# Kernel optimization log

Hardware: AMD Instinct MI355X
Metric: run time of the kernel (lower is better)

Reference implementation:

```python
import jax, jax.numpy as jnp
import numpy as np

B, E, Hh, Ww = 32, 256, 64, 64
HID = 256

def setup_inputs() -> dict:
    key = jax.random.key(0)
    k1, k2, k3 = jax.random.split(key, 3)
    x = jax.random.normal(k1, (B, E, Hh, Ww), dtype=jnp.float32)
    # 1x1 conv weights flattened to [out_ch, in_ch]
    Wqkv = jax.random.normal(k2, (1 + 2 * HID, E), dtype=jnp.float32) * (1.0 / np.sqrt(E))
    bqkv = jnp.zeros((1 + 2 * HID,), dtype=jnp.float32)
    Wout = jax.random.normal(k3, (E, HID), dtype=jnp.float32) * (1.0 / np.sqrt(HID))
    bout = jnp.zeros((E,), dtype=jnp.float32)
    return {"x": x, "Wqkv": Wqkv, "bqkv": bqkv, "Wout": Wout, "bout": bout}

def reference(x, Wqkv, bqkv, Wout, bout):
    hid = HID
    # 1x1 conv == channel-wise matmul: [B,C,H,W] x [O,C] -> [B,O,H,W]
    qkv = jnp.einsum('bchw,oc->bohw', x, Wqkv) + bqkv[None, :, None, None]
    query = qkv[:, :1]               # [B,1,H,W]
    key_t = qkv[:, 1:1 + hid]        # [B,hid,H,W]
    value = qkv[:, 1 + hid:]         # [B,hid,H,W]
    # softmax over the last (width) axis; dropout is identity at eval
    context_scores = jax.nn.softmax(query, axis=-1)
    # softmax-weighted sum over width -> [B,hid,H,1]
    context_vector = jnp.sum(key_t * context_scores, axis=-1, keepdims=True)
    # relu gate on value, broadcast context over width
    gated = jax.nn.relu(value) * context_vector  # [B,hid,H,W]
    out = jnp.einsum('bchw,oc->bohw', gated, Wout) + bout[None, :, None, None]
    return out
```

## Files before the change

kernel.cpp:

```cpp
#include <hip/hip_runtime.h>

#define BB   32
#define EE   256
#define HH   64
#define WW   64
#define HIDN 256

typedef short bf16x8 __attribute__((ext_vector_type(8)));
typedef float f32x4  __attribute__((ext_vector_type(4)));

__device__ __forceinline__ float ubf(unsigned short u) {
  return __uint_as_float(((unsigned)u) << 16);
}
__device__ __forceinline__ unsigned f2bf(float f) {
  unsigned u = __float_as_uint(f);
  u += 0x7fffu + ((u >> 16) & 1u);
  return u >> 16;
}

__device__ __forceinline__ int xt_idx(int w, int c) {
  return (w << 8) + ((((c >> 3) ^ (w & 7)) << 3) | (c & 7));
}

__global__ __launch_bounds__(256) void prep_weights(
    const float* __restrict__ Wqkv, const float* __restrict__ Wout,
    unsigned short* __restrict__ ws)
{
  const int t = blockIdx.x * 256 + threadIdx.x;
  const int which = t >> 13;
  const int r = t & 8191;
  const int m = r >> 5, k8 = r & 31, k0 = k8 * 8;
  const float* src = which ? (Wout + m * HIDN + k0)
                           : (Wqkv + (1 + HIDN + m) * EE + k0);
  unsigned short* dst = ws + which * 131072;
  float4 a = *(const float4*)src;
  float4 bq = *(const float4*)(src + 4);
  float v[8] = {a.x, a.y, a.z, a.w, bq.x, bq.y, bq.z, bq.w};
  const int mt = m >> 4, ks = k8 >> 2, lane = (m & 15) + ((k8 & 3) << 4);
  const int base = ((mt * 8 + ks) * 2) * 64 * 8 + lane * 8;
  __align__(16) unsigned short hs[8], ls[8];
  #pragma unroll
  for (int i = 0; i < 8; ++i) {
    unsigned h = f2bf(v[i]);
    hs[i] = (unsigned short)h;
    ls[i] = (unsigned short)f2bf(v[i] - ubf((unsigned short)h));
  }
  *(uint4*)&dst[base]       = *(const uint4*)hs;
  *(uint4*)&dst[base + 512] = *(const uint4*)ls;
}

__device__ __forceinline__ void mfma_gemm(
    const bf16x8* __restrict__ Wp,
    const unsigned short* __restrict__ Xhp,
    const unsigned short* __restrict__ Xlp,
    const int wid, const int lane, f32x4 acc[4][4])
{
  const int l15 = lane & 15;
  const int kb  = (lane >> 4) * 8;
  #pragma unroll
  for (int ks = 0; ks < 8; ++ks) {
    bf16x8 bhf[4], blf[4];
    #pragma unroll
    for (int ni = 0; ni < 4; ++ni) {
      const int w  = ni * 16 + l15;
      const int c0 = ks * 32 + kb;
      bhf[ni] = *(const bf16x8*)&Xhp[xt_idx(w, c0)];
      blf[ni] = *(const bf16x8*)&Xlp[xt_idx(w, c0)];
    }
    bf16x8 ahf[4], alf[4];
    #pragma unroll
    for (int mi = 0; mi < 4; ++mi) {
      const int fb = ((wid * 4 + mi) * 8 + ks) * 2;
      ahf[mi] = Wp[fb * 64 + lane];
      alf[mi] = Wp[(fb + 1) * 64 + lane];
    }
    #pragma unroll
    for (int mi = 0; mi < 4; ++mi) {
      #pragma unroll
      for (int ni = 0; ni < 4; ++ni) {
        acc[mi][ni] = __builtin_amdgcn_mfma_f32_16x16x32_bf16(ahf[mi], bhf[ni], acc[mi][ni], 0, 0, 0);
        acc[mi][ni] = __builtin_amdgcn_mfma_f32_16x16x32_bf16(ahf[mi], blf[ni], acc[mi][ni], 0, 0, 0);
        acc[mi][ni] = __builtin_amdgcn_mfma_f32_16x16x32_bf16(alf[mi], bhf[ni], acc[mi][ni], 0, 0, 0);
      }
    }
  }
}

__global__ __launch_bounds__(256, 2) void sep_attn_mfma(
    const float* __restrict__ x, const float* __restrict__ Wqkv,
    const float* __restrict__ bqkv, const float* __restrict__ bout,
    float* __restrict__ out, const unsigned short* __restrict__ wsp)
{
  __shared__ __align__(16) unsigned short Xh[64 * 256];
  __shared__ __align__(16) unsigned short Xl[64 * 256];
  __shared__ __align__(16) float qpart[256];
  __shared__ __align__(16) float ss[64];
  __shared__ __align__(16) float xbar_s[EE];
  __shared__ __align__(16) float cvs[EE];
  __shared__ __align__(16) float sbv[EE];
  __shared__ __align__(16) float sbout[EE];

  const int tid  = threadIdx.x;
  const int lane = tid & 63;
  const int wid  = tid >> 6;
  const int bh = blockIdx.x;
  const int b  = bh >> 6;
  const int h  = bh & 63;
  const int gbase = (b * EE) * 4096 + h * 64;

  {
    const int c = tid;
    const float* xp = x + gbase + c * 4096;
    sbv[tid]   = bqkv[1 + HIDN + tid];
    sbout[tid] = bout[tid];
    #pragma unroll
    for (int f = 0; f < 16; ++f) {
      float4 xv = *(const float4*)&xp[f * 4];
      float vv[4] = {xv.x, xv.y, xv.z, xv.w};
      #pragma unroll
      for (int j = 0; j < 4; ++j) {
        const int w = f * 4 + j;
        unsigned hu = f2bf(vv[j]);
        Xh[xt_idx(w, c)] = (unsigned short)hu;
        Xl[xt_idx(w, c)] = (unsigned short)f2bf(vv[j] - ubf((unsigned short)hu));
      }
    }
  }
  __syncthreads();

  {
    const int w = tid & 63, cg = tid >> 6;
    const float* wq = Wqkv + cg * 64;
    float q = 0.f;
    #pragma unroll
    for (int f = 0; f < 8; ++f) {
      const int c0 = cg * 64 + f * 8;
      bf16x8 hv = *(const bf16x8*)&Xh[xt_idx(w, c0)];
      bf16x8 lv = *(const bf16x8*)&Xl[xt_idx(w, c0)];
      float4 wa = *(const float4*)&wq[f * 8];
      float4 wb = *(const float4*)&wq[f * 8 + 4];
      float wf[8] = {wa.x, wa.y, wa.z, wa.w, wb.x, wb.y, wb.z, wb.w};
      #pragma unroll
      for (int e = 0; e < 8; ++e)
        q = fmaf(wf[e], ubf((unsigned short)hv[e]) + ubf((unsigned short)lv[e]), q);
    }
    qpart[tid] = q;
  }
  __syncthreads();

  if (tid < 64) {
    float q = qpart[tid] + qpart[64 + tid] + qpart[128 + tid] + qpart[192 + tid] + bqkv[0];
    float m = q;
    #pragma unroll
    for (int off = 32; off; off >>= 1) m = fmaxf(m, __shfl_xor(m, off));
    float e = expf(q - m);
    float s = e;
    #pragma unroll
    for (int off = 32; off; off >>= 1) s += __shfl_xor(s, off);
    ss[tid] = e / s;
  }
  __syncthreads();

  {
    const int c = tid;
    float a = 0.f;
    #pragma unroll
    for (int f = 0; f < 16; ++f) {
      float4 sv = *(const float4*)&ss[f * 4];
      float4 xv = *(const float4*)&x[gbase + c * 4096 + f * 4];
      a += sv.x * xv.x + sv.y * xv.y + sv.z * xv.z + sv.w * xv.w;
    }
    xbar_s[c] = a;
  }
  __syncthreads();

  {
    const int c = tid;
    const float* wk = Wqkv + (1 + c) * EE;
    float a = 0.f;
    #pragma unroll 8
    for (int f = 0; f < 64; ++f) {
      float4 wv = *(const float4*)&wk[f * 4];
      float4 xb = *(const float4*)&xbar_s[f * 4];
      a += wv.x * xb.x + wv.y * xb.y + wv.z * xb.z + wv.w * xb.w;
    }
    cvs[c] = a + bqkv[1 + c];
  }

  f32x4 acc[4][4];
  #pragma unroll
  for (int mi = 0; mi < 4; ++mi)
    #pragma unroll
    for (int ni = 0; ni < 4; ++ni) {
      acc[mi][ni][0] = 0.f; acc[mi][ni][1] = 0.f;
      acc[mi][ni][2] = 0.f; acc[mi][ni][3] = 0.f;
    }
  mfma_gemm((const bf16x8*)wsp, Xh, Xl, wid, lane, acc);
  __syncthreads();

  {
    const int l15 = lane & 15, l4 = lane >> 4;
    #pragma unroll
    for (int mi = 0; mi < 4; ++mi) {
      const int c0 = (wid * 4 + mi) * 16 + l4 * 4;
      float4 cv4 = *(const float4*)&cvs[c0];
      float4 bv4 = *(const float4*)&sbv[c0];
      float cvv[4] = {cv4.x, cv4.y, cv4.z, cv4.w};
      float bvv[4] = {bv4.x, bv4.y, bv4.z, bv4.w};
      #pragma unroll
      for (int ni = 0; ni < 4; ++ni) {
        const int w = ni * 16 + l15;
        unsigned hs[4], lsv[4];
        #pragma unroll
        for (int rg = 0; rg < 4; ++rg) {
          float g = fmaxf(acc[mi][ni][rg] + bvv[rg], 0.f) * cvv[rg];
          unsigned hu = f2bf(g);
          hs[rg]  = hu;
          lsv[rg] = f2bf(g - ubf((unsigned short)hu));
        }
        uint2 uh, ul;
        uh.x = hs[0]  | (hs[1]  << 16); uh.y = hs[2]  | (hs[3]  << 16);
        ul.x = lsv[0] | (lsv[1] << 16); ul.y = lsv[2] | (lsv[3] << 16);
        *(uint2*)&Xh[xt_idx(w, c0)] = uh;
        *(uint2*)&Xl[xt_idx(w, c0)] = ul;
      }
    }
  }
  __syncthreads();

  #pragma unroll
  for (int mi = 0; mi < 4; ++mi)
    #pragma unroll
    for (int ni = 0; ni < 4; ++ni) {
      acc[mi][ni][0] = 0.f; acc[mi][ni][1] = 0.f;
      acc[mi][ni][2] = 0.f; acc[mi][ni][3] = 0.f;
    }
  mfma_gemm((const bf16x8*)(wsp + 131072), Xh, Xl, wid, lane, acc);

  {
    const int l15 = lane & 15, l4 = lane >> 4;
    #pragma unroll
    for (int mi = 0; mi < 4; ++mi) {
      const int e0 = (wid * 4 + mi) * 16 + l4 * 4;
      float4 bo4 = *(const float4*)&sbout[e0];
      float bov[4] = {bo4.x, bo4.y, bo4.z, bo4.w};
      #pragma unroll
      for (int ni = 0; ni < 4; ++ni) {
        const int w = ni * 16 + l15;
        #pragma unroll
        for (int rg = 0; rg < 4; ++rg)
          out[(b * EE + e0 + rg) * 4096 + h * 64 + w] = acc[mi][ni][rg] + bov[rg];
      }
    }
  }
}

extern "C" void kernel_launch(void* const* d_in, const int* in_sizes, int n_in,
                              void* d_out, int out_size, void* d_ws, size_t ws_size,
                              hipStream_t stream) {
  const float* x    = (const float*)d_in[0];
  const float* Wqkv = (const float*)d_in[1];
  const float* bqkv = (const float*)d_in[2];
  const float* Wout = (const float*)d_in[3];
  const float* bout = (const float*)d_in[4];
  unsigned short* ws = (unsigned short*)d_ws;
  hipLaunchKernelGGL(prep_weights, dim3(64), dim3(256), 0, stream, Wqkv, Wout, ws);
  hipLaunchKernelGGL(sep_attn_mfma, dim3(BB * HH), dim3(256), 0, stream,
                     x, Wqkv, bqkv, bout, (float*)d_out, ws);
}
```

Measured before the change: 381.7 us.

## Switch split-bf16 GEMMs to fp16 with split weights only, drop X low part

Replaces the three-term bf16 hi/lo emulation with fp16, keeping hi/lo splits only for the weights and a single fp16 copy of activations. This cuts MFMA count from three to two per tile and halves the activation LDS footprint, which allows three blocks per CU. It also moves the x load to coalesced float4 reads with a shuffle transpose, reuses the LDS copy for the context reduction instead of rereading global x, and prefetches the next weight fragments with raised wave priority around the MFMA block. The cost is reduced accuracy, since fp16 activations have a limited range and no low-part correction.

```diff
diff --git a/kernel.cpp b/kernel.cpp
--- a/kernel.cpp
+++ b/kernel.cpp
@@ -6,16 +6,15 @@
 #define WW   64
 #define HIDN 256
 
-typedef short bf16x8 __attribute__((ext_vector_type(8)));
-typedef float f32x4  __attribute__((ext_vector_type(4)));
-
-__device__ __forceinline__ float ubf(unsigned short u) {
-  return __uint_as_float(((unsigned)u) << 16);
-}
-__device__ __forceinline__ unsigned f2bf(float f) {
-  unsigned u = __float_as_uint(f);
-  u += 0x7fffu + ((u >> 16) & 1u);
-  return u >> 16;
+typedef _Float16 f16x8 __attribute__((ext_vector_type(8)));
+typedef float    f32x4 __attribute__((ext_vector_type(4)));
+
+__device__ __forceinline__ unsigned f2h(float f) {
+  _Float16 h = (_Float16)f;
+  return (unsigned)__builtin_bit_cast(unsigned short, h);
+}
+__device__ __forceinline__ float h2f(unsigned short u) {
+  return (float)__builtin_bit_cast(_Float16, u);
 }
 
 __device__ __forceinline__ int xt_idx(int w, int c) {
@@ -41,58 +40,72 @@
   __align__(16) unsigned short hs[8], ls[8];
   #pragma unroll
   for (int i = 0; i < 8; ++i) {
-    unsigned h = f2bf(v[i]);
-    hs[i] = (unsigned short)h;
-    ls[i] = (unsigned short)f2bf(v[i] - ubf((unsigned short)h));
+    unsigned hu = f2h(v[i]);
+    hs[i] = (unsigned short)hu;
+    ls[i] = (unsigned short)f2h(v[i] - h2f((unsigned short)hu));
   }
   *(uint4*)&dst[base]       = *(const uint4*)hs;
   *(uint4*)&dst[base + 512] = *(const uint4*)ls;
 }
 
-__device__ __forceinline__ void mfma_gemm(
-    const bf16x8* __restrict__ Wp,
-    const unsigned short* __restrict__ Xhp,
-    const unsigned short* __restrict__ Xlp,
-    const int wid, const int lane, f32x4 acc[4][4])
+__device__ __forceinline__ void preload_a(
+    const f16x8* __restrict__ Wp, int wid, int lane, f16x8 ah[4], f16x8 al[4])
+{
+  #pragma unroll
+  for (int mi = 0; mi < 4; ++mi) {
+    const int fb = ((wid * 4 + mi) * 8) * 2;
+    ah[mi] = Wp[fb * 64 + lane];
+    al[mi] = Wp[(fb + 1) * 64 + lane];
+  }
+}
+
+__device__ __forceinline__ void mfma_gemm_f16(
+    const f16x8* __restrict__ Wp,
+    const unsigned short* __restrict__ Xp,
+    const int wid, const int lane,
+    f16x8 ah[4], f16x8 al[4],
+    f32x4 acc[4][4])
 {
   const int l15 = lane & 15;
   const int kb  = (lane >> 4) * 8;
   #pragma unroll
   for (int ks = 0; ks < 8; ++ks) {
-    bf16x8 bhf[4], blf[4];
-    #pragma unroll
-    for (int ni = 0; ni < 4; ++ni) {
-      const int w  = ni * 16 + l15;
-      const int c0 = ks * 32 + kb;
-      bhf[ni] = *(const bf16x8*)&Xhp[xt_idx(w, c0)];
-      blf[ni] = *(const bf16x8*)&Xlp[xt_idx(w, c0)];
-    }
-    bf16x8 ahf[4], alf[4];
+    f16x8 ahn[4], aln[4];
+    if (ks < 7) {
+      #pragma unroll
+      for (int mi = 0; mi < 4; ++mi) {
+        const int fb = ((wid * 4 + mi) * 8 + ks + 1) * 2;
+        ahn[mi] = Wp[fb * 64 + lane];
+        aln[mi] = Wp[(fb + 1) * 64 + lane];
+      }
+    }
+    f16x8 bf[4];
+    #pragma unroll
+    for (int ni = 0; ni < 4; ++ni)
+      bf[ni] = *(const f16x8*)&Xp[xt_idx(ni * 16 + l15, ks * 32 + kb)];
+    __builtin_amdgcn_s_setprio(1);
     #pragma unroll
     for (int mi = 0; mi < 4; ++mi) {
-      const int fb = ((wid * 4 + mi) * 8 + ks) * 2;
-      ahf[mi] = Wp[fb * 64 + lane];
-      alf[mi] = Wp[(fb + 1) * 64 + lane];
-    }
-    #pragma unroll
-    for (int mi = 0; mi < 4; ++mi) {
       #pragma unroll
       for (int ni = 0; ni < 4; ++ni) {
-        acc[mi][ni] = __builtin_amdgcn_mfma_f32_16x16x32_bf16(ahf[mi], bhf[ni], acc[mi][ni], 0, 0, 0);
-        acc[mi][ni] = __builtin_amdgcn_mfma_f32_16x16x32_bf16(ahf[mi], blf[ni], acc[mi][ni], 0, 0, 0);
-        acc[mi][ni] = __builtin_amdgcn_mfma_f32_16x16x32_bf16(alf[mi], bhf[ni], acc[mi][ni], 0, 0, 0);
-      }
-    }
-  }
-}
-
-__global__ __launch_bounds__(256, 2) void sep_attn_mfma(
+        acc[mi][ni] = __builtin_amdgcn_mfma_f32_16x16x32_f16(ah[mi], bf[ni], acc[mi][ni], 0, 0, 0);
+        acc[mi][ni] = __builtin_amdgcn_mfma_f32_16x16x32_f16(al[mi], bf[ni], acc[mi][ni], 0, 0, 0);
+      }
+    }
+    __builtin_amdgcn_s_setprio(0);
+    if (ks < 7) {
+      #pragma unroll
+      for (int mi = 0; mi < 4; ++mi) { ah[mi] = ahn[mi]; al[mi] = aln[mi]; }
+    }
+  }
+}
+
+__global__ __launch_bounds__(256, 3) void sep_attn_mfma(
     const float* __restrict__ x, const float* __restrict__ Wqkv,
     const float* __restrict__ bqkv, const float* __restrict__ bout,
     float* __restrict__ out, const unsigned short* __restrict__ wsp)
 {
   __shared__ __align__(16) unsigned short Xh[64 * 256];
-  __shared__ __align__(16) unsigned short Xl[64 * 256];
   __shared__ __align__(16) float qpart[256];
   __shared__ __align__(16) float ss[64];
   __shared__ __align__(16) float xbar_s[EE];
@@ -109,24 +122,36 @@
   const int gbase = (b * EE) * 4096 + h * 64;
 
   {
-    const int c = tid;
-    const float* xp = x + gbase + c * 4096;
     sbv[tid]   = bqkv[1 + HIDN + tid];
     sbout[tid] = bout[tid];
-    #pragma unroll
-    for (int f = 0; f < 16; ++f) {
-      float4 xv = *(const float4*)&xp[f * 4];
-      float vv[4] = {xv.x, xv.y, xv.z, xv.w};
-      #pragma unroll
-      for (int j = 0; j < 4; ++j) {
-        const int w = f * 4 + j;
-        unsigned hu = f2bf(vv[j]);
-        Xh[xt_idx(w, c)] = (unsigned short)hu;
-        Xl[xt_idx(w, c)] = (unsigned short)f2bf(vv[j] - ubf((unsigned short)hu));
-      }
-    }
-  }
-  __syncthreads();
+    const int wq = lane & 15, c_off = lane >> 4;
+    const int sel = c_off & 1, sel2 = c_off >> 1;
+    const int wfin = wq * 4 + sel * 2 + sel2;
+    #pragma unroll
+    for (int it = 0; it < 16; ++it) {
+      const int cb = it * 16 + wid * 4;
+      const int c  = cb + c_off;
+      float4 v = *(const float4*)&x[gbase + c * 4096 + wq * 4];
+      unsigned p0 = f2h(v.x) | (f2h(v.y) << 16);
+      unsigned p1 = f2h(v.z) | (f2h(v.w) << 16);
+      unsigned rA = (unsigned)__shfl_xor((int)p0, 16);
+      unsigned rB = (unsigned)__shfl_xor((int)p1, 16);
+      unsigned a_src = sel ? rB : p0;
+      unsigned b_src = sel ? p1 : rA;
+      unsigned d0 = (a_src & 0xffffu) | (b_src << 16);
+      unsigned d1 = (a_src >> 16) | (b_src & 0xffff0000u);
+      unsigned e0 = (unsigned)__shfl_xor((int)d0, 32);
+      unsigned e1 = (unsigned)__shfl_xor((int)d1, 32);
+      uint2 qq;
+      qq.x = sel2 ? e1 : d0;
+      qq.y = sel2 ? d1 : e0;
+      *(uint2*)&Xh[xt_idx(wfin, cb)] = qq;
+    }
+  }
+  __syncthreads();
+
+  f16x8 a1h[4], a1l[4];
+  preload_a((const f16x8*)wsp, wid, lane, a1h, a1l);
 
   {
     const int w = tid & 63, cg = tid >> 6;
@@ -135,14 +160,13 @@
     #pragma unroll
     for (int f = 0; f < 8; ++f) {
       const int c0 = cg * 64 + f * 8;
-      bf16x8 hv = *(const bf16x8*)&Xh[xt_idx(w, c0)];
-      bf16x8 lv = *(const bf16x8*)&Xl[xt_idx(w, c0)];
+      f16x8 hv = *(const f16x8*)&Xh[xt_idx(w, c0)];
       float4 wa = *(const float4*)&wq[f * 8];
       float4 wb = *(const float4*)&wq[f * 8 + 4];
       float wf[8] = {wa.x, wa.y, wa.z, wa.w, wb.x, wb.y, wb.z, wb.w};
       #pragma unroll
       for (int e = 0; e < 8; ++e)
-        q = fmaf(wf[e], ubf((unsigned short)hv[e]) + ubf((unsigned short)lv[e]), q);
+        q = fmaf(wf[e], (float)hv[e], q);
     }
     qpart[tid] = q;
   }
@@ -167,8 +191,10 @@
     #pragma unroll
     for (int f = 0; f < 16; ++f) {
       float4 sv = *(const float4*)&ss[f * 4];
-      float4 xv = *(const float4*)&x[gbase + c * 4096 + f * 4];
-      a += sv.x * xv.x + sv.y * xv.y + sv.z * xv.z + sv.w * xv.w;
+      float svf[4] = {sv.x, sv.y, sv.z, sv.w};
+      #pragma unroll
+      for (int j = 0; j < 4; ++j)
+        a = fmaf(svf[j], h2f(Xh[xt_idx(f * 4 + j, c)]), a);
     }
     xbar_s[c] = a;
   }
@@ -195,7 +221,11 @@
       acc[mi][ni][0] = 0.f; acc[mi][ni][1] = 0.f;
       acc[mi][ni][2] = 0.f; acc[mi][ni][3] = 0.f;
     }
-  mfma_gemm((const bf16x8*)wsp, Xh, Xl, wid, lane, acc);
+  mfma_gemm_f16((const f16x8*)wsp, Xh, wid, lane, a1h, a1l, acc);
+
+  f16x8 a2h[4], a2l[4];
+  preload_a((const f16x8*)(wsp + 131072), wid, lane, a2h, a2l);
+
   __syncthreads();
 
   {
@@ -210,19 +240,14 @@
       #pragma unroll
       for (int ni = 0; ni < 4; ++ni) {
         const int w = ni * 16 + l15;
-        unsigned hs[4], lsv[4];
+        unsigned hs[4];
         #pragma unroll
-        for (int rg = 0; rg < 4; ++rg) {
-          float g = fmaxf(acc[mi][ni][rg] + bvv[rg], 0.f) * cvv[rg];
-          unsigned hu = f2bf(g);
-          hs[rg]  = hu;
-          lsv[rg] = f2bf(g - ubf((unsigned short)hu));
-        }
-        uint2 uh, ul;
-        uh.x = hs[0]  | (hs[1]  << 16); uh.y = hs[2]  | (hs[3]  << 16);
-        ul.x = lsv[0] | (lsv[1] << 16); ul.y = lsv[2] | (lsv[3] << 16);
+        for (int rg = 0; rg < 4; ++rg)
+          hs[rg] = f2h(fmaxf(acc[mi][ni][rg] + bvv[rg], 0.f) * cvv[rg]);
+        uint2 uh;
+        uh.x = hs[0] | (hs[1] << 16);
+        uh.y = hs[2] | (hs[3] << 16);
         *(uint2*)&Xh[xt_idx(w, c0)] = uh;
-        *(uint2*)&Xl[xt_idx(w, c0)] = ul;
       }
     }
   }
@@ -235,7 +260,7 @@
       acc[mi][ni][0] = 0.f; acc[mi][ni][1] = 0.f;
       acc[mi][ni][2] = 0.f; acc[mi][ni][3] = 0.f;
     }
-  mfma_gemm((const bf16x8*)(wsp + 131072), Xh, Xl, wid, lane, acc);
+  mfma_gemm_f16((const f16x8*)(wsp + 131072), Xh, wid, lane, a2h, a2l, acc);
 
   {
     const int l15 = lane & 15, l4 = lane >> 4;
```

Measured after the change: 357.4 us. 1.07x faster.
